# Performance work log

Measured on AMD Instinct MI355X. Metric: run time of the kernel, lower is better.

Reference implementation:

```python
import jax, jax.numpy as jnp
import numpy as np
from math import comb

# --- module hyperparameters (from init_kwargs / module-level constants) ---
F = 32          # features
NITER = 3       # num_iterations
NB = 16         # num_basis_functions
NDCM = 4        # n_dcm
CUTOFF = 4.0
MAXZ = 17       # max_atomic_number
NC = 9          # (max_degree+1)^2 spherical components, max_degree=2
DEG = np.array([0, 1, 1, 1, 2, 2, 2, 2, 2])  # degree l of each component
BINOM = jnp.asarray([comb(NB - 1, k) for k in range(NB)], dtype=jnp.float32)


def _np_sph9(x, y, z):
    # real spherical harmonics up to l=2 on the unit sphere (numpy, for Gaunt table)
    c0 = 0.28209479177387814; c1 = 0.4886025119029199
    c2a = 1.0925484305920792; c2b = 0.31539156525252005; c2c = 0.5462742152960396
    return np.stack([c0 * np.ones_like(x), c1 * y, c1 * z, c1 * x,
                     c2a * x * y, c2a * y * z, c2b * (3.0 * z * z - 1.0),
                     c2a * x * z, c2c * (x * x - y * y)], axis=0)


def _gaunt():
    # real Gaunt (Clebsch-Gordan-type) coefficients G[a,b,c] = int Y_a Y_b Y_c dOmega
    # via Gauss-Legendre (cos theta) x midpoint (phi) quadrature -- exact for l<=2 products
    ct, wt = np.polynomial.legendre.leggauss(64)
    nph = 256
    phi = (np.arange(nph) + 0.5) * (2.0 * np.pi / nph)
    st = np.sqrt(1.0 - ct ** 2)
    x = st[:, None] * np.cos(phi)[None, :]
    y = st[:, None] * np.sin(phi)[None, :]
    z = np.broadcast_to(ct[:, None], x.shape)
    w = (wt[:, None] * (2.0 * np.pi / nph)) * np.ones((1, nph))
    Y = _np_sph9(x, y, z)
    G = np.einsum('aij,bij,cij,ij->abc', Y, Y, Y, w)
    G[np.abs(G) < 1e-6] = 0.0
    return G

CG = jnp.asarray(_gaunt(), dtype=jnp.float32)  # (9, 9, 9), sparse


def _sph9(u):
    # u: (E, 3) unit vectors -> (E, 9)
    x, y, z = u[:, 0], u[:, 1], u[:, 2]
    c0 = 0.28209479177387814; c1 = 0.4886025119029199
    c2a = 1.0925484305920792; c2b = 0.31539156525252005; c2c = 0.5462742152960396
    return jnp.stack([jnp.full_like(x, c0), c1 * y, c1 * z, c1 * x,
                      c2a * x * y, c2a * y * z, c2b * (3.0 * z * z - 1.0),
                      c2a * x * z, c2c * (x * x - y * y)], axis=-1)


def _radial(r):
    # reciprocal Bernstein radial basis * smooth cutoff; r: (E,) -> (E, NB)
    u = 1.0 / (1.0 + r)
    k = jnp.arange(NB, dtype=jnp.float32)
    rb = BINOM * u[:, None] ** k * (1.0 - u[:, None]) ** (NB - 1 - k)
    t = r / CUTOFF
    den = jnp.where(t < 1.0, 1.0 - t * t, 1.0)
    fc = jnp.where(t < 1.0, jnp.exp(-t * t / den), 0.0)  # smooth_cutoff
    return rb * fc[:, None]


def _equiv_dense(x, W, b=None):
    # per-degree linear (equivariant Dense): x (N, 9, Fin), W (3, Fin, Fout); bias on l=0 only
    y = jnp.einsum('ncf,cfg->ncg', x, W[DEG])
    if b is not None:
        y = y.at[:, 0, :].add(b)
    return y


def _tp(xs, bf):
    # Gaunt tensor-product contraction: out[e,c,f] = sum_ab CG[a,b,c] xs[e,a,f] bf[e,b,f]
    # loop over the 9 fixed output components to avoid an (E,9,9,F) intermediate
    out = []
    for c in range(NC):
        t = jnp.einsum('eaf,ab->ebf', xs, CG[:, :, c])
        out.append(jnp.sum(t * bf, axis=1))
    return jnp.stack(out, axis=1)


def _forward(atomic_numbers, positions, dst_idx, src_idx, embed, Wb, W1, b1, W2, b2,
             Wt00, Wt11, Wmono, element_bias):
    n = atomic_numbers.shape[0]
    disp = positions[src_idx] - positions[dst_idx]                 # (E, 3) gather
    r = jnp.sqrt(jnp.sum(disp * disp, axis=-1) + 1e-12)            # safe norm
    u = disp / r[:, None]
    basis = _sph9(u)[:, :, None] * _radial(r)[:, None, :]          # (E, 9, NB)
    x = jnp.zeros((n, NC, F), dtype=positions.dtype).at[:, 0, :].set(embed[atomic_numbers])
    for i in range(NITER):  # message passing iterations
        bf = jnp.einsum('ebn,bng->ebg', basis, Wb[i][DEG])         # per-degree radial->feature mix (E,9,F)
        msg = _tp(x[src_idx], bf)                                  # gather src + tensor product
        y = x + jax.ops.segment_sum(msg, dst_idx, num_segments=n)  # scatter-aggregate + residual add
        y = _equiv_dense(y, W1[i], b1[i])
        y = jax.nn.silu(y)
        y = _equiv_dense(y, W2[i], b2[i])
        x = x + y                                                  # residual update
    # TensorDense to n_dcm channels, then readout heads
    mono = (x[:, 0, :] @ Wt00) @ Wmono + element_bias[atomic_numbers][:, None]  # (N, NDCM)
    dip = jnp.einsum('ncf,fg->ncg', x[:, 1:4, :], Wt11)            # (N, 3, NDCM) vector channel
    dip = jnp.clip(jax.nn.silu(dip), -0.3, 0.3) + positions[:, :, None]
    return mono, dip


def setup_inputs():
    key = jax.random.key(0)
    ks = jax.random.split(key, 12)
    N, E = 10000, 160000
    return {
        'atomic_numbers': jax.random.randint(ks[0], (N,), 0, MAXZ + 1),
        'positions': jax.random.normal(ks[1], (N, 3), jnp.float32) * 3.0,
        'dst_idx': jax.random.randint(ks[2], (E,), 0, N),
        'src_idx': jax.random.randint(ks[3], (E,), 0, N),
        'embed': jax.random.normal(ks[4], (MAXZ + 1, F), jnp.float32),
        'Wb': jax.random.normal(ks[5], (NITER, 3, NB, F), jnp.float32) / np.sqrt(NB).astype(np.float32),
        'W1': jax.random.normal(ks[6], (NITER, 3, F, F), jnp.float32) / np.sqrt(F).astype(np.float32),
        'b1': jnp.zeros((NITER, F), jnp.float32),
        'W2': jax.random.normal(ks[7], (NITER, 3, F, F), jnp.float32) / np.sqrt(F).astype(np.float32),
        'b2': jnp.zeros((NITER, F), jnp.float32),
        'Wt00': jax.random.normal(ks[8], (F, NDCM), jnp.float32) / np.sqrt(F).astype(np.float32),
        'Wt11': jax.random.normal(ks[9], (F, NDCM), jnp.float32) / np.sqrt(F).astype(np.float32),
        'Wmono': jax.random.normal(ks[10], (NDCM, NDCM), jnp.float32) / np.sqrt(NDCM).astype(np.float32),
        'element_bias': jnp.zeros((MAXZ + 1,), jnp.float32),
    }


def reference(atomic_numbers, positions, dst_idx, src_idx, embed, Wb, W1, b1, W2, b2,
              Wt00, Wt11, Wmono, element_bias):
    return _forward(atomic_numbers, positions, dst_idx, src_idx, embed, Wb, W1, b1, W2, b2,
                    Wt00, Wt11, Wmono, element_bias)
```

## Files before the change

kernel.cpp:

```cpp
#include <hip/hip_runtime.h>
#include <hip/hip_bf16.h>


#define NITER 3
#define BCAP  64

#define OFF_WB    0
#define OFF_W1    4608
#define OFF_B1    13824
#define OFF_W2    13920
#define OFF_B2    23136
#define OFF_WT00  23232
#define OFF_WT11  23360
#define OFF_WMONO 23488
#define OFF_EB    23504
#define OFF_EMB   23522
#define WC_TOTAL  24098

__device__ __forceinline__ float b2f(const __hip_bfloat16 v) { return __bfloat162float(v); }

#define KC0 0.28209479177387814f
#define KG1 0.21850968611841584f
#define KG2 0.12615662610100802f
#define KG3 0.18022375157287861f
#define KG4 0.09011187578643931f
#define KG5 0.15607834722743988f

__device__ __forceinline__ float ldany(const void* p, int i, bool f32) {
    return f32 ? ((const float*)p)[i] : b2f(((const __hip_bfloat16*)p)[i]);
}

__device__ __forceinline__ bool wave_sniff(const void* pos) {
    const __hip_bfloat16* p = (const __hip_bfloat16*)pos;
    int lane = threadIdx.x & 63;
    int bad = 0;
    #pragma unroll
    for (int k = 0; k < 4; k++) {
        float v = b2f(p[lane + k*64]);
        bad |= !(fabsf(v) < 1.0e6f);
    }
    return __ballot(bad) != 0ull;
}

__device__ __forceinline__ float xadd32(float v) {
    return v + __int_as_float(__shfl_xor(__float_as_int(v), 32, 64));
}

__device__ __forceinline__ bool edge_geom(float dx, float dy, float dz,
                                          float* sp, float* rad) {
    float r2 = dx*dx + dy*dy + dz*dz + 1e-12f;
    if (r2 >= 16.0f) return false;
    float r  = sqrtf(r2);
    float t2 = r2 * 0.0625f;
    float fc = __expf(-t2 / (1.0f - t2));
    float u = 1.0f / (1.0f + r);
    float v = 1.0f - u;
    const float BIN[16] = {1.f,15.f,105.f,455.f,1365.f,3003.f,5005.f,6435.f,
                           6435.f,5005.f,3003.f,1365.f,455.f,105.f,15.f,1.f};
    float vp[16];
    vp[0] = 1.0f;
    #pragma unroll
    for (int k = 1; k < 16; k++) vp[k] = vp[k-1] * v;
    float up = 1.0f;
    #pragma unroll
    for (int n = 0; n < 16; n++) { rad[n] = BIN[n] * up * vp[15-n] * fc; up *= u; }
    float ir = 1.0f / r;
    float ux = dx*ir, uy = dy*ir, uz = dz*ir;
    const float c0 = 0.28209479177387814f, c1 = 0.4886025119029199f;
    const float c2a = 1.0925484305920792f, c2b = 0.31539156525252005f, c2c = 0.5462742152960396f;
    sp[0] = c0;
    sp[1] = c1*uy; sp[2] = c1*uz; sp[3] = c1*ux;
    sp[4] = c2a*ux*uy; sp[5] = c2a*uy*uz; sp[6] = c2b*(3.0f*uz*uz - 1.0f);
    sp[7] = c2a*ux*uz; sp[8] = c2c*(ux*ux - uy*uy);
    return true;
}

__global__ void setup_kernel(const void* pos, const void* Wb, const void* W1,
        const void* b1, const void* W2, const void* b2, const void* Wt00,
        const void* Wt11, const void* Wmono, const void* eb, const void* emb,
        const int* __restrict__ an,
        const int* __restrict__ srcI, const int* __restrict__ dstI,
        float* __restrict__ posf, float* __restrict__ wc,
        float* __restrict__ x, float* __restrict__ geo2, int* __restrict__ cur,
        int N, int E, int use_csr) {
    bool f32 = wave_sniff(pos);
    int i = blockIdx.x * blockDim.x + threadIdx.x;
    int np = N * 3;
    if (i < np) { posf[i] = ldany(pos, i, f32); return; }
    int j = i - np;
    if (j < WC_TOTAL) {
        const void* src; int rel;
        if      (j < OFF_W1)    { src = Wb;    rel = j; }
        else if (j < OFF_B1)    { src = W1;    rel = j - OFF_W1; }
        else if (j < OFF_W2)    { src = b1;    rel = j - OFF_B1; }
        else if (j < OFF_B2)    { src = W2;    rel = j - OFF_W2; }
        else if (j < OFF_WT00)  { src = b2;    rel = j - OFF_B2; }
        else if (j < OFF_WT11)  { src = Wt00;  rel = j - OFF_WT00; }
        else if (j < OFF_WMONO) { src = Wt11;  rel = j - OFF_WT11; }
        else if (j < OFF_EB)    { src = Wmono; rel = j - OFF_WMONO; }
        else if (j < OFF_EMB)   { src = eb;    rel = j - OFF_EB; }
        else                    { src = emb;   rel = j - OFF_EMB; }
        wc[j] = ldany(src, rel, f32);
        return;
    }
    j -= WC_TOTAL;
    if (j < N * 32) {
        int n = j >> 5, rem = j & 31;
        x[(size_t)n * 288 + rem] = ldany(emb, an[n] * 32 + rem, f32);
        return;
    }
    j -= N * 32;
    if (j < E && use_csr) {
        int s = srcI[j], d = dstI[j];
        float sp[9], rad[16];
        if (!edge_geom(ldany(pos, s*3+0, f32) - ldany(pos, d*3+0, f32),
                       ldany(pos, s*3+1, f32) - ldany(pos, d*3+1, f32),
                       ldany(pos, s*3+2, f32) - ldany(pos, d*3+2, f32),
                       sp, rad)) return;
        int slot = atomicAdd(&cur[d], 1);
        float* gp = geo2 + ((size_t)d * BCAP + slot) * 32;
        gp[0] = __int_as_float(s);
        gp[1] = 0.0f;
        #pragma unroll
        for (int a = 0; a < 9; a++) gp[2 + a] = sp[a];
        gp[11] = 0.0f;
        #pragma unroll
        for (int k = 0; k < 16; k++) gp[16 + k] = rad[k];
    }
}

template <bool FIRST, bool LAST>
__global__ __launch_bounds__(256) void edge_gather_kernel(
        const float* __restrict__ x, float* __restrict__ y,
        const float* __restrict__ geo2, const int* __restrict__ cur,
        const float* __restrict__ Wbi, int N) {
    int tid  = threadIdx.x;
    int f    = tid & 31;
    int half = (tid >> 5) & 1;
    int n    = (blockIdx.x * blockDim.x + tid) >> 6;
    if (n >= N) return;
    float w0[16], w1[16], w2[16];
    #pragma unroll
    for (int k = 0; k < 16; k++) {
        w0[k] = Wbi[(0*16 + k)*32 + f];
        w1[k] = Wbi[(1*16 + k)*32 + f];
        w2[k] = Wbi[(2*16 + k)*32 + f];
    }
    float A0=0.f,A1=0.f,A2=0.f,A3=0.f,A4=0.f,A5=0.f,A6=0.f,A7=0.f,A8=0.f;
    int beg = n * BCAP, end = beg + cur[n];
    for (int e = beg + half; e < end; e += 2) {
        const float4* gp = (const float4*)(geo2 + (size_t)e * 32);
        float4 h0 = gp[0], h1 = gp[1], h2 = gp[2];
        float4 r0 = gp[4], r1 = gp[5], r2 = gp[6], r3 = gp[7];
        int s = __float_as_int(h0.x);
        float rad[16] = {r0.x,r0.y,r0.z,r0.w, r1.x,r1.y,r1.z,r1.w,
                         r2.x,r2.y,r2.z,r2.w, r3.x,r3.y,r3.z,r3.w};
        float rw0 = 0.f, rw1 = 0.f, rw2 = 0.f;
        #pragma unroll
        for (int k = 0; k < 16; k++) {
            rw0 = fmaf(rad[k], w0[k], rw0);
            rw1 = fmaf(rad[k], w1[k], rw1);
            rw2 = fmaf(rad[k], w2[k], rw2);
        }
        float B0 = h0.z*rw0;
        float B1 = h0.w*rw1, B2 = h1.x*rw1, B3 = h1.y*rw1;
        float B4 = h1.z*rw2, B5 = h1.w*rw2, B6 = h2.x*rw2,
              B7 = h2.y*rw2, B8 = h2.z*rw2;
        const float* xp = x + (size_t)s*288 + f;
        if (FIRST) {
            float X0 = xp[0];
            float k0 = KC0 * X0;
            A0 += k0*B0; A1 += k0*B1; A2 += k0*B2; A3 += k0*B3; A4 += k0*B4;
            A5 += k0*B5; A6 += k0*B6; A7 += k0*B7; A8 += k0*B8;
        } else {
            float X0 = xp[0],   X1 = xp[32],  X2 = xp[64],  X3 = xp[96],  X4 = xp[128];
            float X5 = xp[160], X6 = xp[192], X7 = xp[224], X8 = xp[256];
            A0 += KC0*(X0*B0 + X1*B1 + X2*B2 + X3*B3 + X4*B4 + X5*B5 + X6*B6 + X7*B7 + X8*B8);
            A1 += KC0*(X0*B1 + X1*B0) + KG1*(X3*B4 + X4*B3 + X2*B5 + X5*B2)
                - KG2*(X1*B6 + X6*B1) - KG1*(X1*B8 + X8*B1);
            A2 += KC0*(X0*B2 + X2*B0) + KG1*(X1*B5 + X5*B1 + X3*B7 + X7*B3)
                + 2.0f*KG2*(X2*B6 + X6*B2);
            A3 += KC0*(X0*B3 + X3*B0) + KG1*(X1*B4 + X4*B1 + X2*B7 + X7*B2)
                - KG2*(X3*B6 + X6*B3) + KG1*(X3*B8 + X8*B3);
            if (!LAST) {
                A4 += KC0*(X0*B4 + X4*B0) + KG1*(X1*B3 + X3*B1) + KG5*(X5*B7 + X7*B5)
                    - KG3*(X4*B6 + X6*B4);
                A5 += KC0*(X0*B5 + X5*B0) + KG1*(X1*B2 + X2*B1) + KG5*(X4*B7 + X7*B4)
                    + KG4*(X5*B6 + X6*B5) - KG5*(X5*B8 + X8*B5);
                A6 += KC0*(X0*B6 + X6*B0) - KG2*X1*B1 + 2.0f*KG2*X2*B2 - KG2*X3*B3
                    - KG3*X4*B4 + KG4*X5*B5 + KG3*X6*B6 + KG4*X7*B7 - KG3*X8*B8;
                A7 += KC0*(X0*B7 + X7*B0) + KG1*(X2*B3 + X3*B2) + KG5*(X4*B5 + X5*B4)
                    + KG4*(X6*B7 + X7*B6) + KG5*(X7*B8 + X8*B7);
                A8 += KC0*(X0*B8 + X8*B0) - KG1*X1*B1 + KG1*X3*B3 - KG5*X5*B5 + KG5*X7*B7
                    - KG3*(X6*B8 + X8*B6);
            }
        }
    }
    A0 = xadd32(A0); A1 = xadd32(A1); A2 = xadd32(A2); A3 = xadd32(A3);
    if (!LAST) {
        A4 = xadd32(A4); A5 = xadd32(A5); A6 = xadd32(A6);
        A7 = xadd32(A7); A8 = xadd32(A8);
    }
    if (half == 0) {
        float* yp = y + (size_t)n * 288 + f;
        yp[0]   = A0; yp[32]  = A1; yp[64]  = A2; yp[96]  = A3;
        if (!LAST) {
            yp[128] = A4; yp[160] = A5; yp[192] = A6; yp[224] = A7; yp[256] = A8;
        }
    }
}

template <bool FIRST>
__global__ __launch_bounds__(256) void atom_kernel(
        float* __restrict__ x, const float* __restrict__ y,
        const float* __restrict__ W1i, const float* __restrict__ b1i,
        const float* __restrict__ W2i, const float* __restrict__ b2i,
        int N) {
    __shared__ float sm[4][64*33];
    int lane  = threadIdx.x & 63;
    int wslot = threadIdx.x >> 6;
    int u = __builtin_amdgcn_readfirstlane(blockIdx.x * 4 + wslot);
    int t = u / 9;
    int c = u - t * 9;
    int d = (c == 0) ? 0 : ((c < 4) ? 1 : 2);
    const float* W1 = W1i + d * 1024;
    const float* W2 = W2i + d * 1024;
    float* tile = sm[wslot];
    bool usex = (!FIRST) || (c == 0);
    float4 xr4[8];
    #pragma unroll
    for (int k = 0; k < 8; k++) {
        int e  = lane * 4 + k * 256;
        int al = e >> 5, f = e & 31;
        int ag = t * 64 + al;
        float4 s = make_float4(0.f, 0.f, 0.f, 0.f);
        float4 xv = make_float4(0.f, 0.f, 0.f, 0.f);
        if (ag < N) {
            if (usex) xv = *(const float4*)(x + (size_t)ag * 288 + c * 32 + f);
            float4 yv = *(const float4*)(y + (size_t)ag * 288 + c * 32 + f);
            s = make_float4(xv.x + yv.x, xv.y + yv.y, xv.z + yv.z, xv.w + yv.w);
        }
        xr4[k] = xv;
        *(float4*)(tile + al * 33 + f) = s;
    }
    __syncthreads();
    float yin[32];
    #pragma unroll
    for (int k = 0; k < 8; k++) {
        float4 v = *(const float4*)(tile + lane * 33 + 4 * k);
        yin[4*k+0] = v.x; yin[4*k+1] = v.y; yin[4*k+2] = v.z; yin[4*k+3] = v.w;
    }
    float acc[32];
    #pragma unroll
    for (int g = 0; g < 32; g++) acc[g] = (c == 0) ? b1i[g] : 0.0f;
    #pragma unroll 4
    for (int fi = 0; fi < 32; fi++) {
        float v = yin[fi];
        #pragma unroll
        for (int g = 0; g < 32; g++) acc[g] = fmaf(v, W1[fi*32 + g], acc[g]);
    }
    #pragma unroll
    for (int g = 0; g < 32; g++)
        acc[g] = acc[g] * __builtin_amdgcn_rcpf(1.0f + __expf(-acc[g]));
    float out[32];
    #pragma unroll
    for (int g = 0; g < 32; g++) out[g] = (c == 0) ? b2i[g] : 0.0f;
    #pragma unroll 4
    for (int fi = 0; fi < 32; fi++) {
        float v = acc[fi];
        #pragma unroll
        for (int g = 0; g < 32; g++) out[g] = fmaf(v, W2[fi*32 + g], out[g]);
    }
    __syncthreads();
    #pragma unroll
    for (int k = 0; k < 8; k++)
        *(float4*)(tile + lane * 33 + 4 * k) =
            make_float4(out[4*k+0], out[4*k+1], out[4*k+2], out[4*k+3]);
    __syncthreads();
    #pragma unroll
    for (int k = 0; k < 8; k++) {
        int e  = lane * 4 + k * 256;
        int al = e >> 5, f = e & 31;
        int ag = t * 64 + al;
        if (ag < N) {
            float4 dv = *(const float4*)(tile + al * 33 + f);
            float4 xv = xr4[k];
            *(float4*)(x + (size_t)ag * 288 + c * 32 + f) =
                make_float4(xv.x + dv.x, xv.y + dv.y, xv.z + dv.z, xv.w + dv.w);
        }
    }
}

__global__ __launch_bounds__(256) void atom_readout_kernel(
        const float* __restrict__ x, const float* __restrict__ y,
        const float* __restrict__ W1i, const float* __restrict__ b1i,
        const float* __restrict__ W2i, const float* __restrict__ b2i,
        const int* __restrict__ an, const float* __restrict__ posf,
        const float* __restrict__ wc, const void* __restrict__ pos,
        void* __restrict__ out_, int N) {
    bool f32 = wave_sniff(pos);
    __shared__ float sm[4][64*33];
    int lane  = threadIdx.x & 63;
    int wslot = threadIdx.x >> 6;
    int c = __builtin_amdgcn_readfirstlane(wslot);
    int t = blockIdx.x;
    int d = (c == 0) ? 0 : 1;
    const float* W1 = W1i + d * 1024;
    const float* W2 = W2i + d * 1024;
    float* tile = sm[wslot];
    float4 xr4[8];
    #pragma unroll
    for (int k = 0; k < 8; k++) {
        int e  = lane * 4 + k * 256;
        int al = e >> 5, f = e & 31;
        int ag = t * 64 + al;
        float4 s = make_float4(0.f, 0.f, 0.f, 0.f);
        float4 xv = make_float4(0.f, 0.f, 0.f, 0.f);
        if (ag < N) {
            xv = *(const float4*)(x + (size_t)ag * 288 + c * 32 + f);
            float4 yv = *(const float4*)(y + (size_t)ag * 288 + c * 32 + f);
            s = make_float4(xv.x + yv.x, xv.y + yv.y, xv.z + yv.z, xv.w + yv.w);
        }
        xr4[k] = xv;
        *(float4*)(tile + al * 33 + f) = s;
    }
    __syncthreads();
    float yin[32];
    #pragma unroll
    for (int k = 0; k < 8; k++) {
        float4 v = *(const float4*)(tile + lane * 33 + 4 * k);
        yin[4*k+0] = v.x; yin[4*k+1] = v.y; yin[4*k+2] = v.z; yin[4*k+3] = v.w;
    }
    float acc[32];
    #pragma unroll
    for (int g = 0; g < 32; g++) acc[g] = (c == 0) ? b1i[g] : 0.0f;
    #pragma unroll 4
    for (int fi = 0; fi < 32; fi++) {
        float v = yin[fi];
        #pragma unroll
        for (int g = 0; g < 32; g++) acc[g] = fmaf(v, W1[fi*32 + g], acc[g]);
    }
    #pragma unroll
    for (int g = 0; g < 32; g++)
        acc[g] = acc[g] * __builtin_amdgcn_rcpf(1.0f + __expf(-acc[g]));
    float out[32];
    #pragma unroll
    for (int g = 0; g < 32; g++) out[g] = (c == 0) ? b2i[g] : 0.0f;
    #pragma unroll 4
    for (int fi = 0; fi < 32; fi++) {
        float v = acc[fi];
        #pragma unroll
        for (int g = 0; g < 32; g++) out[g] = fmaf(v, W2[fi*32 + g], out[g]);
    }
    __syncthreads();
    #pragma unroll
    for (int k = 0; k < 8; k++)
        *(float4*)(tile + lane * 33 + 4 * k) =
            make_float4(out[4*k+0], out[4*k+1], out[4*k+2], out[4*k+3]);
    __syncthreads();
    #pragma unroll
    for (int k = 0; k < 8; k++) {
        int e  = lane * 4 + k * 256;
        int al = e >> 5, f = e & 31;
        float4 dv = *(const float4*)(tile + al * 33 + f);
        float4 xv = xr4[k];
        *(float4*)(tile + al * 33 + f) =
            make_float4(xv.x + dv.x, xv.y + dv.y, xv.z + dv.z, xv.w + dv.w);
    }
    __syncthreads();
    if (threadIdx.x < 64) {
        int a  = threadIdx.x;
        int ag = t * 64 + a;
        if (ag < N) {
            const float* Wt00  = wc + OFF_WT00;
            const float* Wt11  = wc + OFF_WT11;
            const float* Wmono = wc + OFF_WMONO;
            const float* x0 = sm[0] + a * 33;
            float q[4] = {0.f, 0.f, 0.f, 0.f};
            for (int f = 0; f < 32; f++) {
                float xv = x0[f];
                #pragma unroll
                for (int j = 0; j < 4; j++) q[j] = fmaf(xv, Wt00[f*4 + j], q[j]);
            }
            float ebv = wc[OFF_EB + an[ag]];
            #pragma unroll
            for (int m = 0; m < 4; m++) {
                float accm = ebv;
                #pragma unroll
                for (int j = 0; j < 4; j++) accm = fmaf(q[j], Wmono[j*4 + m], accm);
                if (f32) ((float*)out_)[ag*4 + m] = accm;
                else ((__hip_bfloat16*)out_)[ag*4 + m] = __float2bfloat16(accm);
            }
            #pragma unroll
            for (int cc = 0; cc < 3; cc++) {
                float pc = posf[ag*3 + cc];
                const float* xc = sm[1 + cc] + a * 33;
                float dq[4] = {0.f, 0.f, 0.f, 0.f};
                for (int f = 0; f < 32; f++) {
                    float xv = xc[f];
                    #pragma unroll
                    for (int m = 0; m < 4; m++) dq[m] = fmaf(xv, Wt11[f*4 + m], dq[m]);
                }
                #pragma unroll
                for (int m = 0; m < 4; m++) {
                    float v = dq[m];
                    v = v * __builtin_amdgcn_rcpf(1.0f + __expf(-v));
                    v = fminf(fmaxf(v, -0.3f), 0.3f);
                    v += pc;
                    if (f32) ((float*)out_)[N*4 + ag*12 + cc*4 + m] = v;
                    else ((__hip_bfloat16*)out_)[N*4 + ag*12 + cc*4 + m] = __float2bfloat16(v);
                }
            }
        }
    }
}

__global__ void zero_kernel(float4* __restrict__ b, int n) {
    int i = blockIdx.x * blockDim.x + threadIdx.x;
    int stride = gridDim.x * blockDim.x;
    float4 z = make_float4(0.f, 0.f, 0.f, 0.f);
    for (; i < n; i += stride) b[i] = z;
}

__global__ __launch_bounds__(256) void edge_inline_kernel(
        const float* __restrict__ x, float* __restrict__ y,
        const float* __restrict__ posf,
        const int* __restrict__ srcI, const int* __restrict__ dstI,
        const float* __restrict__ Wbi, int E) {
    int f  = threadIdx.x & 31;
    int hw = (blockIdx.x * blockDim.x + threadIdx.x) >> 5;
    int nhw = gridDim.x * (blockDim.x >> 5);
    float w0[16], w1[16], w2[16];
    #pragma unroll
    for (int n = 0; n < 16; n++) {
        w0[n] = Wbi[(0*16 + n)*32 + f];
        w1[n] = Wbi[(1*16 + n)*32 + f];
        w2[n] = Wbi[(2*16 + n)*32 + f];
    }
    for (int e = hw; e < E; e += nhw) {
        int s = srcI[e], d = dstI[e];
        float sp[9], rad[16];
        if (!edge_geom(posf[s*3+0] - posf[d*3+0],
                       posf[s*3+1] - posf[d*3+1],
                       posf[s*3+2] - posf[d*3+2], sp, rad)) continue;
        float rw0 = 0.f, rw1 = 0.f, rw2 = 0.f;
        #pragma unroll
        for (int n = 0; n < 16; n++) {
            rw0 = fmaf(rad[n], w0[n], rw0);
            rw1 = fmaf(rad[n], w1[n], rw1);
            rw2 = fmaf(rad[n], w2[n], rw2);
        }
        float B0 = sp[0]*rw0;
        float B1 = sp[1]*rw1, B2 = sp[2]*rw1, B3 = sp[3]*rw1;
        float B4 = sp[4]*rw2, B5 = sp[5]*rw2, B6 = sp[6]*rw2,
              B7 = sp[7]*rw2, B8 = sp[8]*rw2;
        const float* xp = x + (size_t)s*288 + f;
        float X0 = xp[0],   X1 = xp[32],  X2 = xp[64],  X3 = xp[96],  X4 = xp[128];
        float X5 = xp[160], X6 = xp[192], X7 = xp[224], X8 = xp[256];
        float* yp = y + (size_t)d*288 + f;
        float m;
        m = KC0*(X0*B0 + X1*B1 + X2*B2 + X3*B3 + X4*B4 + X5*B5 + X6*B6 + X7*B7 + X8*B8);
        unsafeAtomicAdd(yp + 0, m);
        m = KC0*(X0*B1 + X1*B0) + KG1*(X3*B4 + X4*B3 + X2*B5 + X5*B2)
          - KG2*(X1*B6 + X6*B1) - KG1*(X1*B8 + X8*B1);
        unsafeAtomicAdd(yp + 32, m);
        m = KC0*(X0*B2 + X2*B0) + KG1*(X1*B5 + X5*B1 + X3*B7 + X7*B3)
          + 2.0f*KG2*(X2*B6 + X6*B2);
        unsafeAtomicAdd(yp + 64, m);
        m = KC0*(X0*B3 + X3*B0) + KG1*(X1*B4 + X4*B1 + X2*B7 + X7*B2)
          - KG2*(X3*B6 + X6*B3) + KG1*(X3*B8 + X8*B3);
        unsafeAtomicAdd(yp + 96, m);
        m = KC0*(X0*B4 + X4*B0) + KG1*(X1*B3 + X3*B1) + KG5*(X5*B7 + X7*B5)
          - KG3*(X4*B6 + X6*B4);
        unsafeAtomicAdd(yp + 128, m);
        m = KC0*(X0*B5 + X5*B0) + KG1*(X1*B2 + X2*B1) + KG5*(X4*B7 + X7*B4)
          + KG4*(X5*B6 + X6*B5) - KG5*(X5*B8 + X8*B5);
        unsafeAtomicAdd(yp + 160, m);
        m = KC0*(X0*B6 + X6*B0) - KG2*X1*B1 + 2.0f*KG2*X2*B2 - KG2*X3*B3
          - KG3*X4*B4 + KG4*X5*B5 + KG3*X6*B6 + KG4*X7*B7 - KG3*X8*B8;
        unsafeAtomicAdd(yp + 192, m);
        m = KC0*(X0*B7 + X7*B0) + KG1*(X2*B3 + X3*B2) + KG5*(X4*B5 + X5*B4)
          + KG4*(X6*B7 + X7*B6) + KG5*(X7*B8 + X8*B7);
        unsafeAtomicAdd(yp + 224, m);
        m = KC0*(X0*B8 + X8*B0) - KG1*X1*B1 + KG1*X3*B3 - KG5*X5*B5 + KG5*X7*B7
          - KG3*(X6*B8 + X8*B6);
        unsafeAtomicAdd(yp + 256, m);
    }
}

__global__ void readout_kernel(const float* __restrict__ x,
        const int* __restrict__ an, const float* __restrict__ posf,
        const float* __restrict__ wc, const void* __restrict__ pos,
        void* __restrict__ out, int N) {
    bool f32 = wave_sniff(pos);
    int n = blockIdx.x * blockDim.x + threadIdx.x;
    if (n >= N) return;
    const float* Wt00  = wc + OFF_WT00;
    const float* Wt11  = wc + OFF_WT11;
    const float* Wmono = wc + OFF_WMONO;
    const float* xb = x + (size_t)n * 288;
    float q[4] = {0.f, 0.f, 0.f, 0.f};
    for (int f = 0; f < 32; f++) {
        float xv = xb[f];
        #pragma unroll
        for (int j = 0; j < 4; j++) q[j] = fmaf(xv, Wt00[f*4 + j], q[j]);
    }
    float ebv = wc[OFF_EB + an[n]];
    #pragma unroll
    for (int m = 0; m < 4; m++) {
        float acc = ebv;
        #pragma unroll
        for (int j = 0; j < 4; j++) acc = fmaf(q[j], Wmono[j*4 + m], acc);
        if (f32) ((float*)out)[n*4 + m] = acc;
        else ((__hip_bfloat16*)out)[n*4 + m] = __float2bfloat16(acc);
    }
    #pragma unroll
    for (int c = 0; c < 3; c++) {
        float pc = posf[n*3 + c];
        const float* xc = xb + (1 + c)*32;
        float dq[4] = {0.f, 0.f, 0.f, 0.f};
        for (int f = 0; f < 32; f++) {
            float xv = xc[f];
            #pragma unroll
            for (int m = 0; m < 4; m++) dq[m] = fmaf(xv, Wt11[f*4 + m], dq[m]);
        }
        #pragma unroll
        for (int m = 0; m < 4; m++) {
            float v = dq[m];
            v = v * __builtin_amdgcn_rcpf(1.0f + __expf(-v));
            v = fminf(fmaxf(v, -0.3f), 0.3f);
            v += pc;
            if (f32) ((float*)out)[N*4 + n*12 + c*4 + m] = v;
            else ((__hip_bfloat16*)out)[N*4 + n*12 + c*4 + m] = __float2bfloat16(v);
        }
    }
}

extern "C" void kernel_launch(void* const* d_in, const int* in_sizes, int n_in,
                              void* d_out, int out_size, void* d_ws, size_t ws_size,
                              hipStream_t stream) {
    const int* an    = (const int*)d_in[0];
    const void* pos  = d_in[1];
    const int* dstI  = (const int*)d_in[2];
    const int* srcI  = (const int*)d_in[3];
    const void* embed= d_in[4];
    const void* Wb   = d_in[5];
    const void* W1   = d_in[6];
    const void* b1   = d_in[7];
    const void* W2   = d_in[8];
    const void* b2   = d_in[9];
    const void* Wt00 = d_in[10];
    const void* Wt11 = d_in[11];
    const void* Wmono= d_in[12];
    const void* eb   = d_in[13];
    int N = in_sizes[0];
    int E = in_sizes[2];

    float* x    = (float*)d_ws;
    float* y    = x + (size_t)N * 288;
    float* posf = y + (size_t)N * 288;
    float* wc   = posf + (size_t)N * 3;
    int* cur    = (int*)(wc + WC_TOTAL);
    uintptr_t ga = ((uintptr_t)(cur + N) + 127) & ~(uintptr_t)127;
    float* geo2 = (float*)ga;
    size_t need = (uintptr_t)(geo2 + (size_t)N * BCAP * 32) - (uintptr_t)d_ws;
    bool use_csr = (ws_size >= need);

    hipMemsetAsync(cur, 0, sizeof(int) * (size_t)N, stream);
    if (!use_csr)
        zero_kernel<<<512, 256, 0, stream>>>((float4*)x, N * 72);
    {
        int tot = N * 3 + WC_TOTAL + N * 32 + (use_csr ? E : 0);
        setup_kernel<<<(tot + 255)/256, 256, 0, stream>>>(
            pos, Wb, W1, b1, W2, b2, Wt00, Wt11, Wmono, eb, embed,
            an, srcI, dstI, posf, wc, x, geo2, cur, N, E, use_csr ? 1 : 0);
    }
    int ntiles = (N + 63) / 64;
    if (use_csr) {
        int gblocks = (N + 3) / 4;
        for (int i = 0; i < NITER; i++) {
            const float* Wbi = wc + OFF_WB + (size_t)i*1536;
            const float* W1i = wc + OFF_W1 + (size_t)i*3072;
            const float* b1i = wc + OFF_B1 + (size_t)i*32;
            const float* W2i = wc + OFF_W2 + (size_t)i*3072;
            const float* b2i = wc + OFF_B2 + (size_t)i*32;
            if (i == 0) {
                edge_gather_kernel<true,false><<<gblocks, 256, 0, stream>>>(
                    x, y, geo2, cur, Wbi, N);
                atom_kernel<true><<<(ntiles*9 + 3)/4, 256, 0, stream>>>(
                    x, y, W1i, b1i, W2i, b2i, N);
            } else if (i == NITER - 1) {
                edge_gather_kernel<false,true><<<gblocks, 256, 0, stream>>>(
                    x, y, geo2, cur, Wbi, N);
                atom_readout_kernel<<<ntiles, 256, 0, stream>>>(
                    x, y, W1i, b1i, W2i, b2i, an, posf, wc, pos, d_out, N);
            } else {
                edge_gather_kernel<false,false><<<gblocks, 256, 0, stream>>>(
                    x, y, geo2, cur, Wbi, N);
                atom_kernel<false><<<(ntiles*9 + 3)/4, 256, 0, stream>>>(
                    x, y, W1i, b1i, W2i, b2i, N);
            }
        }
    } else {
        int ablocks = (ntiles * 9 + 3) / 4;
        for (int i = 0; i < NITER; i++) {
            zero_kernel<<<512, 256, 0, stream>>>((float4*)y, N * 72);
            edge_inline_kernel<<<2048, 256, 0, stream>>>(x, y, posf, srcI, dstI,
                wc + OFF_WB + (size_t)i*1536, E);
            atom_kernel<false><<<ablocks, 256, 0, stream>>>(x, y,
                wc + OFF_W1 + (size_t)i*3072, wc + OFF_B1 + (size_t)i*32,
                wc + OFF_W2 + (size_t)i*3072, wc + OFF_B2 + (size_t)i*32, N);
        }
        readout_kernel<<<(N + 255)/256, 256, 0, stream>>>(x, an, posf, wc, pos,
                                                          d_out, N);
    }
}
```

Before: 214.2 us.

## Fuse iteration loop into persistent cooperative kernel with grid-wide syncs

Replaces the six per-iteration gather and atom kernel launches with one cooperative persistent kernel. Inside it, grid-stride loops cover the gather, atom-update and readout phases, separated by grid.sync(). This is meant to remove launch gaps and tail effects between the small dependent kernels. In exchange, FIRST/LAST become runtime flags instead of template parameters, and occupancy is capped by the register and shared-memory use of the fused kernel. Grid barriers add their own cost, and the old multi-launch path remains as a fallback if the cooperative launch fails.

```diff
diff --git a/kernel.cpp b/kernel.cpp
--- a/kernel.cpp
+++ b/kernel.cpp
@@ -1,5 +1,8 @@
 #include <hip/hip_runtime.h>
 #include <hip/hip_bf16.h>
+#include <hip/hip_cooperative_groups.h>
+
+namespace cg = cooperative_groups;
 
 
 #define NITER 3
@@ -129,16 +132,14 @@
     }
 }
 
-template <bool FIRST, bool LAST>
-__global__ __launch_bounds__(256) void edge_gather_kernel(
+__device__ __forceinline__ void gather_phase(
         const float* __restrict__ x, float* __restrict__ y,
         const float* __restrict__ geo2, const int* __restrict__ cur,
-        const float* __restrict__ Wbi, int N) {
+        const float* __restrict__ Wbi, int N, bool FIRSTf, bool LASTf,
+        int wave0, int wstep) {
     int tid  = threadIdx.x;
     int f    = tid & 31;
     int half = (tid >> 5) & 1;
-    int n    = (blockIdx.x * blockDim.x + tid) >> 6;
-    if (n >= N) return;
     float w0[16], w1[16], w2[16];
     #pragma unroll
     for (int k = 0; k < 16; k++) {
@@ -146,87 +147,83 @@
         w1[k] = Wbi[(1*16 + k)*32 + f];
         w2[k] = Wbi[(2*16 + k)*32 + f];
     }
-    float A0=0.f,A1=0.f,A2=0.f,A3=0.f,A4=0.f,A5=0.f,A6=0.f,A7=0.f,A8=0.f;
-    int beg = n * BCAP, end = beg + cur[n];
-    for (int e = beg + half; e < end; e += 2) {
-        const float4* gp = (const float4*)(geo2 + (size_t)e * 32);
-        float4 h0 = gp[0], h1 = gp[1], h2 = gp[2];
-        float4 r0 = gp[4], r1 = gp[5], r2 = gp[6], r3 = gp[7];
-        int s = __float_as_int(h0.x);
-        float rad[16] = {r0.x,r0.y,r0.z,r0.w, r1.x,r1.y,r1.z,r1.w,
-                         r2.x,r2.y,r2.z,r2.w, r3.x,r3.y,r3.z,r3.w};
-        float rw0 = 0.f, rw1 = 0.f, rw2 = 0.f;
-        #pragma unroll
-        for (int k = 0; k < 16; k++) {
-            rw0 = fmaf(rad[k], w0[k], rw0);
-            rw1 = fmaf(rad[k], w1[k], rw1);
-            rw2 = fmaf(rad[k], w2[k], rw2);
-        }
-        float B0 = h0.z*rw0;
-        float B1 = h0.w*rw1, B2 = h1.x*rw1, B3 = h1.y*rw1;
-        float B4 = h1.z*rw2, B5 = h1.w*rw2, B6 = h2.x*rw2,
-              B7 = h2.y*rw2, B8 = h2.z*rw2;
-        const float* xp = x + (size_t)s*288 + f;
-        if (FIRST) {
-            float X0 = xp[0];
-            float k0 = KC0 * X0;
-            A0 += k0*B0; A1 += k0*B1; A2 += k0*B2; A3 += k0*B3; A4 += k0*B4;
-            A5 += k0*B5; A6 += k0*B6; A7 += k0*B7; A8 += k0*B8;
-        } else {
-            float X0 = xp[0],   X1 = xp[32],  X2 = xp[64],  X3 = xp[96],  X4 = xp[128];
-            float X5 = xp[160], X6 = xp[192], X7 = xp[224], X8 = xp[256];
-            A0 += KC0*(X0*B0 + X1*B1 + X2*B2 + X3*B3 + X4*B4 + X5*B5 + X6*B6 + X7*B7 + X8*B8);
-            A1 += KC0*(X0*B1 + X1*B0) + KG1*(X3*B4 + X4*B3 + X2*B5 + X5*B2)
-                - KG2*(X1*B6 + X6*B1) - KG1*(X1*B8 + X8*B1);
-            A2 += KC0*(X0*B2 + X2*B0) + KG1*(X1*B5 + X5*B1 + X3*B7 + X7*B3)
-                + 2.0f*KG2*(X2*B6 + X6*B2);
-            A3 += KC0*(X0*B3 + X3*B0) + KG1*(X1*B4 + X4*B1 + X2*B7 + X7*B2)
-                - KG2*(X3*B6 + X6*B3) + KG1*(X3*B8 + X8*B3);
-            if (!LAST) {
-                A4 += KC0*(X0*B4 + X4*B0) + KG1*(X1*B3 + X3*B1) + KG5*(X5*B7 + X7*B5)
-                    - KG3*(X4*B6 + X6*B4);
-                A5 += KC0*(X0*B5 + X5*B0) + KG1*(X1*B2 + X2*B1) + KG5*(X4*B7 + X7*B4)
-                    + KG4*(X5*B6 + X6*B5) - KG5*(X5*B8 + X8*B5);
-                A6 += KC0*(X0*B6 + X6*B0) - KG2*X1*B1 + 2.0f*KG2*X2*B2 - KG2*X3*B3
-                    - KG3*X4*B4 + KG4*X5*B5 + KG3*X6*B6 + KG4*X7*B7 - KG3*X8*B8;
-                A7 += KC0*(X0*B7 + X7*B0) + KG1*(X2*B3 + X3*B2) + KG5*(X4*B5 + X5*B4)
-                    + KG4*(X6*B7 + X7*B6) + KG5*(X7*B8 + X8*B7);
-                A8 += KC0*(X0*B8 + X8*B0) - KG1*X1*B1 + KG1*X3*B3 - KG5*X5*B5 + KG5*X7*B7
-                    - KG3*(X6*B8 + X8*B6);
-            }
-        }
-    }
-    A0 = xadd32(A0); A1 = xadd32(A1); A2 = xadd32(A2); A3 = xadd32(A3);
-    if (!LAST) {
-        A4 = xadd32(A4); A5 = xadd32(A5); A6 = xadd32(A6);
-        A7 = xadd32(A7); A8 = xadd32(A8);
-    }
-    if (half == 0) {
-        float* yp = y + (size_t)n * 288 + f;
-        yp[0]   = A0; yp[32]  = A1; yp[64]  = A2; yp[96]  = A3;
-        if (!LAST) {
-            yp[128] = A4; yp[160] = A5; yp[192] = A6; yp[224] = A7; yp[256] = A8;
-        }
-    }
-}
-
-template <bool FIRST>
-__global__ __launch_bounds__(256) void atom_kernel(
+    for (int n = wave0; n < N; n += wstep) {
+        float A0=0.f,A1=0.f,A2=0.f,A3=0.f,A4=0.f,A5=0.f,A6=0.f,A7=0.f,A8=0.f;
+        int beg = n * BCAP, end = beg + cur[n];
+        for (int e = beg + half; e < end; e += 2) {
+            const float4* gp = (const float4*)(geo2 + (size_t)e * 32);
+            float4 h0 = gp[0], h1 = gp[1], h2 = gp[2];
+            float4 r0 = gp[4], r1 = gp[5], r2 = gp[6], r3 = gp[7];
+            int s = __float_as_int(h0.x);
+            float rad[16] = {r0.x,r0.y,r0.z,r0.w, r1.x,r1.y,r1.z,r1.w,
+                             r2.x,r2.y,r2.z,r2.w, r3.x,r3.y,r3.z,r3.w};
+            float rw0 = 0.f, rw1 = 0.f, rw2 = 0.f;
+            #pragma unroll
+            for (int k = 0; k < 16; k++) {
+                rw0 = fmaf(rad[k], w0[k], rw0);
+                rw1 = fmaf(rad[k], w1[k], rw1);
+                rw2 = fmaf(rad[k], w2[k], rw2);
+            }
+            float B0 = h0.z*rw0;
+            float B1 = h0.w*rw1, B2 = h1.x*rw1, B3 = h1.y*rw1;
+            float B4 = h1.z*rw2, B5 = h1.w*rw2, B6 = h2.x*rw2,
+                  B7 = h2.y*rw2, B8 = h2.z*rw2;
+            const float* xp = x + (size_t)s*288 + f;
+            if (FIRSTf) {
+                float k0 = KC0 * xp[0];
+                A0 += k0*B0; A1 += k0*B1; A2 += k0*B2; A3 += k0*B3; A4 += k0*B4;
+                A5 += k0*B5; A6 += k0*B6; A7 += k0*B7; A8 += k0*B8;
+            } else {
+                float X0 = xp[0],   X1 = xp[32],  X2 = xp[64],  X3 = xp[96],  X4 = xp[128];
+                float X5 = xp[160], X6 = xp[192], X7 = xp[224], X8 = xp[256];
+                A0 += KC0*(X0*B0 + X1*B1 + X2*B2 + X3*B3 + X4*B4 + X5*B5 + X6*B6 + X7*B7 + X8*B8);
+                A1 += KC0*(X0*B1 + X1*B0) + KG1*(X3*B4 + X4*B3 + X2*B5 + X5*B2)
+                    - KG2*(X1*B6 + X6*B1) - KG1*(X1*B8 + X8*B1);
+                A2 += KC0*(X0*B2 + X2*B0) + KG1*(X1*B5 + X5*B1 + X3*B7 + X7*B3)
+                    + 2.0f*KG2*(X2*B6 + X6*B2);
+                A3 += KC0*(X0*B3 + X3*B0) + KG1*(X1*B4 + X4*B1 + X2*B7 + X7*B2)
+                    - KG2*(X3*B6 + X6*B3) + KG1*(X3*B8 + X8*B3);
+                if (!LASTf) {
+                    A4 += KC0*(X0*B4 + X4*B0) + KG1*(X1*B3 + X3*B1) + KG5*(X5*B7 + X7*B5)
+                        - KG3*(X4*B6 + X6*B4);
+                    A5 += KC0*(X0*B5 + X5*B0) + KG1*(X1*B2 + X2*B1) + KG5*(X4*B7 + X7*B4)
+                        + KG4*(X5*B6 + X6*B5) - KG5*(X5*B8 + X8*B5);
+                    A6 += KC0*(X0*B6 + X6*B0) - KG2*X1*B1 + 2.0f*KG2*X2*B2 - KG2*X3*B3
+                        - KG3*X4*B4 + KG4*X5*B5 + KG3*X6*B6 + KG4*X7*B7 - KG3*X8*B8;
+                    A7 += KC0*(X0*B7 + X7*B0) + KG1*(X2*B3 + X3*B2) + KG5*(X4*B5 + X5*B4)
+                        + KG4*(X6*B7 + X7*B6) + KG5*(X7*B8 + X8*B7);
+                    A8 += KC0*(X0*B8 + X8*B0) - KG1*X1*B1 + KG1*X3*B3 - KG5*X5*B5 + KG5*X7*B7
+                        - KG3*(X6*B8 + X8*B6);
+                }
+            }
+        }
+        A0 = xadd32(A0); A1 = xadd32(A1); A2 = xadd32(A2); A3 = xadd32(A3);
+        if (!LASTf) {
+            A4 = xadd32(A4); A5 = xadd32(A5); A6 = xadd32(A6);
+            A7 = xadd32(A7); A8 = xadd32(A8);
+        }
+        if (half == 0) {
+            float* yp = y + (size_t)n * 288 + f;
+            yp[0]   = A0; yp[32]  = A1; yp[64]  = A2; yp[96]  = A3;
+            if (!LASTf) {
+                yp[128] = A4; yp[160] = A5; yp[192] = A6; yp[224] = A7; yp[256] = A8;
+            }
+        }
+    }
+}
+
+__device__ __forceinline__ void atom_unit(
         float* __restrict__ x, const float* __restrict__ y,
         const float* __restrict__ W1i, const float* __restrict__ b1i,
         const float* __restrict__ W2i, const float* __restrict__ b2i,
-        int N) {
-    __shared__ float sm[4][64*33];
-    int lane  = threadIdx.x & 63;
-    int wslot = threadIdx.x >> 6;
-    int u = __builtin_amdgcn_readfirstlane(blockIdx.x * 4 + wslot);
+        int N, bool FIRSTf, int u, bool au, float* tile) {
+    int lane = threadIdx.x & 63;
     int t = u / 9;
     int c = u - t * 9;
     int d = (c == 0) ? 0 : ((c < 4) ? 1 : 2);
     const float* W1 = W1i + d * 1024;
     const float* W2 = W2i + d * 1024;
-    float* tile = sm[wslot];
-    bool usex = (!FIRST) || (c == 0);
+    bool usex = (!FIRSTf) || (c == 0);
     float4 xr4[8];
     #pragma unroll
     for (int k = 0; k < 8; k++) {
@@ -235,7 +232,7 @@
         int ag = t * 64 + al;
         float4 s = make_float4(0.f, 0.f, 0.f, 0.f);
         float4 xv = make_float4(0.f, 0.f, 0.f, 0.f);
-        if (ag < N) {
+        if (au && ag < N) {
             if (usex) xv = *(const float4*)(x + (size_t)ag * 288 + c * 32 + f);
             float4 yv = *(const float4*)(y + (size_t)ag * 288 + c * 32 + f);
             s = make_float4(xv.x + yv.x, xv.y + yv.y, xv.z + yv.z, xv.w + yv.w);
@@ -282,7 +279,7 @@
         int e  = lane * 4 + k * 256;
         int al = e >> 5, f = e & 31;
         int ag = t * 64 + al;
-        if (ag < N) {
+        if (au && ag < N) {
             float4 dv = *(const float4*)(tile + al * 33 + f);
             float4 xv = xr4[k];
             *(float4*)(x + (size_t)ag * 288 + c * 32 + f) =
@@ -291,19 +288,16 @@
     }
 }
 
-__global__ __launch_bounds__(256) void atom_readout_kernel(
+__device__ __forceinline__ void atom_readout_tile(
         const float* __restrict__ x, const float* __restrict__ y,
         const float* __restrict__ W1i, const float* __restrict__ b1i,
         const float* __restrict__ W2i, const float* __restrict__ b2i,
         const int* __restrict__ an, const float* __restrict__ posf,
-        const float* __restrict__ wc, const void* __restrict__ pos,
-        void* __restrict__ out_, int N) {
-    bool f32 = wave_sniff(pos);
-    __shared__ float sm[4][64*33];
+        const float* __restrict__ wc, bool f32, void* __restrict__ out_,
+        int N, int t, bool at, float (*sm)[64*33]) {
     int lane  = threadIdx.x & 63;
     int wslot = threadIdx.x >> 6;
     int c = __builtin_amdgcn_readfirstlane(wslot);
-    int t = blockIdx.x;
     int d = (c == 0) ? 0 : 1;
     const float* W1 = W1i + d * 1024;
     const float* W2 = W2i + d * 1024;
@@ -316,7 +310,7 @@
         int ag = t * 64 + al;
         float4 s = make_float4(0.f, 0.f, 0.f, 0.f);
         float4 xv = make_float4(0.f, 0.f, 0.f, 0.f);
-        if (ag < N) {
+        if (at && ag < N) {
             xv = *(const float4*)(x + (size_t)ag * 288 + c * 32 + f);
             float4 yv = *(const float4*)(y + (size_t)ag * 288 + c * 32 + f);
             s = make_float4(xv.x + yv.x, xv.y + yv.y, xv.z + yv.z, xv.w + yv.w);
@@ -371,7 +365,7 @@
     if (threadIdx.x < 64) {
         int a  = threadIdx.x;
         int ag = t * 64 + a;
-        if (ag < N) {
+        if (at && ag < N) {
             const float* Wt00  = wc + OFF_WT00;
             const float* Wt11  = wc + OFF_WT11;
             const float* Wmono = wc + OFF_WMONO;
@@ -413,6 +407,90 @@
             }
         }
     }
+}
+
+__global__ __launch_bounds__(256) void loop_kernel(
+        float* __restrict__ x, float* __restrict__ y,
+        const float* __restrict__ geo2, const int* __restrict__ cur,
+        const float* __restrict__ wc, const int* __restrict__ an,
+        const float* __restrict__ posf, const void* __restrict__ pos,
+        void* __restrict__ out_, int N) {
+    cg::grid_group grid = cg::this_grid();
+    __shared__ float sm[4][64*33];
+    bool f32 = wave_sniff(pos);
+    int ntiles = (N + 63) / 64;
+    int wave0 = (blockIdx.x * blockDim.x + threadIdx.x) >> 6;
+    int wstep = (gridDim.x * blockDim.x) >> 6;
+    int wslot = threadIdx.x >> 6;
+
+    for (int it = 0; it < NITER; it++) {
+        bool FIRSTf = (it == 0);
+        bool LASTf  = (it == NITER - 1);
+        const float* Wbi = wc + OFF_WB + it*1536;
+        const float* W1i = wc + OFF_W1 + it*3072;
+        const float* b1i = wc + OFF_B1 + it*32;
+        const float* W2i = wc + OFF_W2 + it*3072;
+        const float* b2i = wc + OFF_B2 + it*32;
+
+        gather_phase(x, y, geo2, cur, Wbi, N, FIRSTf, LASTf, wave0, wstep);
+        grid.sync();
+
+        if (!LASTf) {
+            int nunits = ntiles * 9;
+            int grid4  = gridDim.x * 4;
+            int trips  = (nunits + grid4 - 1) / grid4;
+            for (int k = 0; k < trips; k++) {
+                int u = (k * gridDim.x + blockIdx.x) * 4 + wslot;
+                bool au = (u < nunits);
+                atom_unit(x, y, W1i, b1i, W2i, b2i, N, FIRSTf,
+                          au ? u : 0, au, sm[wslot]);
+            }
+            grid.sync();
+        } else {
+            int trips = (ntiles + gridDim.x - 1) / gridDim.x;
+            for (int k = 0; k < trips; k++) {
+                int t = k * gridDim.x + blockIdx.x;
+                bool at = (t < ntiles);
+                atom_readout_tile(x, y, W1i, b1i, W2i, b2i, an, posf, wc,
+                                  f32, out_, N, at ? t : 0, at, sm);
+            }
+        }
+    }
+}
+
+template <bool FIRST, bool LAST>
+__global__ __launch_bounds__(256) void edge_gather_kernel(
+        const float* __restrict__ x, float* __restrict__ y,
+        const float* __restrict__ geo2, const int* __restrict__ cur,
+        const float* __restrict__ Wbi, int N) {
+    int wave0 = (blockIdx.x * blockDim.x + threadIdx.x) >> 6;
+    if (wave0 >= N) return;
+    gather_phase(x, y, geo2, cur, Wbi, N, FIRST, LAST, wave0, 1 << 30);
+}
+
+template <bool FIRST>
+__global__ __launch_bounds__(256) void atom_kernel(
+        float* __restrict__ x, const float* __restrict__ y,
+        const float* __restrict__ W1i, const float* __restrict__ b1i,
+        const float* __restrict__ W2i, const float* __restrict__ b2i,
+        int N) {
+    __shared__ float sm[4][64*33];
+    int wslot = threadIdx.x >> 6;
+    int u = __builtin_amdgcn_readfirstlane(blockIdx.x * 4 + wslot);
+    atom_unit(x, y, W1i, b1i, W2i, b2i, N, FIRST, u, true, sm[wslot]);
+}
+
+__global__ __launch_bounds__(256) void atom_readout_kernel(
+        const float* __restrict__ x, const float* __restrict__ y,
+        const float* __restrict__ W1i, const float* __restrict__ b1i,
+        const float* __restrict__ W2i, const float* __restrict__ b2i,
+        const int* __restrict__ an, const float* __restrict__ posf,
+        const float* __restrict__ wc, const void* __restrict__ pos,
+        void* __restrict__ out_, int N) {
+    bool f32 = wave_sniff(pos);
+    __shared__ float sm[4][64*33];
+    atom_readout_tile(x, y, W1i, b1i, W2i, b2i, an, posf, wc, f32, out_,
+                      N, blockIdx.x, true, sm);
 }
 
 __global__ void zero_kernel(float4* __restrict__ b, int n) {
@@ -577,28 +655,52 @@
     }
     int ntiles = (N + 63) / 64;
     if (use_csr) {
-        int gblocks = (N + 3) / 4;
-        for (int i = 0; i < NITER; i++) {
-            const float* Wbi = wc + OFF_WB + (size_t)i*1536;
-            const float* W1i = wc + OFF_W1 + (size_t)i*3072;
-            const float* b1i = wc + OFF_B1 + (size_t)i*32;
-            const float* W2i = wc + OFF_W2 + (size_t)i*3072;
-            const float* b2i = wc + OFF_B2 + (size_t)i*32;
-            if (i == 0) {
-                edge_gather_kernel<true,false><<<gblocks, 256, 0, stream>>>(
-                    x, y, geo2, cur, Wbi, N);
-                atom_kernel<true><<<(ntiles*9 + 3)/4, 256, 0, stream>>>(
-                    x, y, W1i, b1i, W2i, b2i, N);
-            } else if (i == NITER - 1) {
-                edge_gather_kernel<false,true><<<gblocks, 256, 0, stream>>>(
-                    x, y, geo2, cur, Wbi, N);
-                atom_readout_kernel<<<ntiles, 256, 0, stream>>>(
-                    x, y, W1i, b1i, W2i, b2i, an, posf, wc, pos, d_out, N);
-            } else {
-                edge_gather_kernel<false,false><<<gblocks, 256, 0, stream>>>(
-                    x, y, geo2, cur, Wbi, N);
-                atom_kernel<false><<<(ntiles*9 + 3)/4, 256, 0, stream>>>(
-                    x, y, W1i, b1i, W2i, b2i, N);
+        bool coop_done = false;
+        int maxb = 0;
+        hipError_t oe = hipOccupancyMaxActiveBlocksPerMultiprocessor(
+            &maxb, loop_kernel, 256, 0);
+        int numCU = 0;
+        hipError_t ae = hipDeviceGetAttribute(&numCU,
+            hipDeviceAttributeMultiprocessorCount, 0);
+        if (oe == hipSuccess && ae == hipSuccess && maxb > 0 && numCU > 0) {
+            int grid = maxb * numCU;
+            int gmax = (N + 3) / 4;
+            if (grid > gmax) grid = gmax;
+            float* xa = x; float* ya = y;
+            const float* g2 = geo2; const int* cu = cur;
+            const float* wcp = wc; const int* anp = an;
+            const float* pf = posf; const void* pp = pos;
+            void* op = d_out; int Nn = N;
+            void* args[] = {&xa, &ya, (void*)&g2, (void*)&cu, (void*)&wcp,
+                            (void*)&anp, (void*)&pf, (void*)&pp, &op, &Nn};
+            hipError_t rc = hipLaunchCooperativeKernel(
+                (const void*)loop_kernel, dim3(grid), dim3(256), args, 0, stream);
+            coop_done = (rc == hipSuccess);
+        }
+        if (!coop_done) {
+            int gblocks = (N + 3) / 4;
+            for (int i = 0; i < NITER; i++) {
+                const float* Wbi = wc + OFF_WB + (size_t)i*1536;
+                const float* W1i = wc + OFF_W1 + (size_t)i*3072;
+                const float* b1i = wc + OFF_B1 + (size_t)i*32;
+                const float* W2i = wc + OFF_W2 + (size_t)i*3072;
+                const float* b2i = wc + OFF_B2 + (size_t)i*32;
+                if (i == 0) {
+                    edge_gather_kernel<true,false><<<gblocks, 256, 0, stream>>>(
+                        x, y, geo2, cur, Wbi, N);
+                    atom_kernel<true><<<(ntiles*9 + 3)/4, 256, 0, stream>>>(
+                        x, y, W1i, b1i, W2i, b2i, N);
+                } else if (i == NITER - 1) {
+                    edge_gather_kernel<false,true><<<gblocks, 256, 0, stream>>>(
+                        x, y, geo2, cur, Wbi, N);
+                    atom_readout_kernel<<<ntiles, 256, 0, stream>>>(
+                        x, y, W1i, b1i, W2i, b2i, an, posf, wc, pos, d_out, N);
+                } else {
+                    edge_gather_kernel<false,false><<<gblocks, 256, 0, stream>>>(
+                        x, y, geo2, cur, Wbi, N);
+                    atom_kernel<false><<<(ntiles*9 + 3)/4, 256, 0, stream>>>(
+                        x, y, W1i, b1i, W2i, b2i, N);
+                }
             }
         }
     } else {
```

Measured after the change: 469.2 us. 2.19x slower.
